# Optimization experiments

Hardware: AMD Instinct MI355X
Metric: run time of the kernel (lower is better)

The kernel has to match this reference:

```python
import jax, jax.numpy as jnp
import numpy as np

PI = 3.141592653589793

# ---------------- smoothing-constant solvers (numpy, import time) -------------
# Quadratic smoothing b*(r-rc)^2 matched to value V and slope dV at r.
def _smooth(V, dV, r):
    rc = r - 2.0 * V / dV
    b = dV * dV / (4.0 * V)
    return float(b), float(rc)

def _f1c(a, r0, rc, rlow, rhigh):  # smoothed Morse (stacking / hbond radial)
    shift = (1.0 - np.exp(-a * (rc - r0))) ** 2
    def V(r):
        return (1.0 - np.exp(-a * (r - r0))) ** 2 - shift
    def dV(r):
        e = np.exp(-a * (r - r0))
        return 2.0 * (1.0 - e) * a * e
    blow, rclow = _smooth(V(rlow), dV(rlow), rlow)
    bhigh, rchigh = _smooth(V(rhigh), dV(rhigh), rhigh)
    return dict(a=a, r0=r0, shift=float(shift), rlow=rlow, rhigh=rhigh,
                blow=blow, rclow=rclow, bhigh=bhigh, rchigh=rchigh)

def _f2c(k, r0, rc, rlow, rhigh):  # smoothed harmonic well (cross/coaxial radial)
    dc2 = (rc - r0) ** 2
    def V(r):
        return 0.5 * k * ((r - r0) ** 2 - dc2)
    def dV(r):
        return k * (r - r0)
    blow, rclow = _smooth(V(rlow), dV(rlow), rlow)
    bhigh, rchigh = _smooth(V(rhigh), dV(rhigh), rhigh)
    return dict(k=k, r0=r0, dc2=float(dc2), rlow=rlow, rhigh=rhigh,
                blow=blow, rclow=rclow, bhigh=bhigh, rchigh=rchigh)

def _f3c(sigma, rstar):  # smoothed LJ excluded volume
    s6 = sigma ** 6
    V = 4.0 * (s6 * s6 / rstar ** 12 - s6 / rstar ** 6)
    dV = 4.0 * (-12.0 * s6 * s6 / rstar ** 13 + 6.0 * s6 / rstar ** 7)
    b, rc = _smooth(V, dV, rstar)
    return dict(sigma=sigma, rstar=rstar, b=b, rc=rc)

def _f4c(a, t0, ts):  # smoothed angular modulation 1-a*(th-t0)^2
    b = a * a * ts * ts / (1.0 - a * ts * ts)
    tc = ts + a * ts / b
    return dict(a=a, t0=t0, ts=ts, b=float(b), tc=float(tc))

def _f5c(a, xs):  # one-sided smoothed modulation on a cosine
    V = 1.0 - a * xs * xs
    dV = -2.0 * a * xs
    xc = xs - 2.0 * V / dV
    b = dV * dV / (4.0 * V)
    return dict(a=a, xs=xs, xc=float(xc), b=float(b))

FENE_EPS, FENE_R0, FENE_DELTA = 2.0, 0.7525, 0.25
F1_STCK = _f1c(6.0, 0.4, 0.9, 0.32, 0.75)
F1_HB = _f1c(8.0, 0.4, 0.75, 0.34, 0.70)
F2_CRST = _f2c(47.5, 0.575, 0.675, 0.495, 0.655)
F2_CX = _f2c(46.0, 0.4, 0.6, 0.22, 0.58)
F3_BACK = _f3c(0.70, 0.675)
F3_BASE = _f3c(0.33, 0.32)
F3_MIX = _f3c(0.515, 0.50)
F4 = dict(
    s4=_f4c(1.30, 0.0, 0.80), s5=_f4c(0.90, 0.0, 0.95), s6=_f4c(0.90, 0.0, 0.95),
    h1=_f4c(1.50, 0.0, 0.70), h2=_f4c(1.50, 0.0, 0.70), h3=_f4c(1.50, 0.0, 0.70),
    h4=_f4c(0.46, PI, 0.70), h7=_f4c(4.00, 0.5 * PI, 0.45), h8=_f4c(4.00, 0.5 * PI, 0.45),
    c1=_f4c(2.25, 0.791, 0.58), c2=_f4c(1.70, 1.003, 0.68), c3=_f4c(1.70, 1.003, 0.68),
    c4=_f4c(1.50, 0.0, 0.70), c7=_f4c(1.70, 0.555, 0.68), c8=_f4c(1.70, 0.555, 0.68),
    x1=_f4c(2.00, 2.592, 0.65), x4=_f4c(1.30, 0.0, 0.80))
F5C = _f5c(2.0, -0.65)
POS_BACK, POS_STACK, POS_BASE = -0.4, 0.34, 0.4

# ---------------- jnp piecewise potential pieces ------------------------------
def f1(r, c):
    e = jnp.exp(-c['a'] * (r - c['r0']))
    core = (1.0 - e) ** 2 - c['shift']
    v = jnp.where(r < c['rlow'], c['blow'] * (r - c['rclow']) ** 2,
        jnp.where(r < c['rhigh'], core, c['bhigh'] * (r - c['rchigh']) ** 2))
    return jnp.where((r > c['rclow']) & (r < c['rchigh']), v, 0.0)

def f2(r, c):
    core = 0.5 * c['k'] * ((r - c['r0']) ** 2 - c['dc2'])
    v = jnp.where(r < c['rlow'], c['blow'] * (r - c['rclow']) ** 2,
        jnp.where(r < c['rhigh'], core, c['bhigh'] * (r - c['rchigh']) ** 2))
    return jnp.where((r > c['rclow']) & (r < c['rchigh']), v, 0.0)

def f3(r, c, eps):
    x6 = (c['sigma'] / r) ** 6
    lj = 4.0 * (x6 * x6 - x6)
    v = jnp.where(r < c['rstar'], lj, c['b'] * (r - c['rc']) ** 2)
    return eps * jnp.where(r < c['rc'], v, 0.0)

def f4(theta, c):
    dt = jnp.abs(theta - c['t0'])
    v = jnp.where(dt < c['ts'], 1.0 - c['a'] * dt * dt, c['b'] * (c['tc'] - dt) ** 2)
    return jnp.where(dt < c['tc'], v, 0.0)

def f5(x, c):
    v = jnp.where(x > c['xs'], 1.0 - c['a'] * x * x, c['b'] * (c['xc'] - x) ** 2)
    v = jnp.where(x > 0.0, 1.0, v)
    return jnp.where(x > c['xc'], v, 0.0)

# ---------------- geometry helpers --------------------------------------------
def quat_axes(q):  # rotation-matrix rows a1,a2,a3, each (N,3)
    w, x, y, z = q[..., 0], q[..., 1], q[..., 2], q[..., 3]
    a1 = jnp.stack([w*w + x*x - y*y - z*z, 2*(x*y + w*z), 2*(x*z - w*y)], -1)
    a2 = jnp.stack([2*(x*y - w*z), w*w - x*x + y*y - z*z, 2*(y*z + w*x)], -1)
    a3 = jnp.stack([2*(x*z + w*y), 2*(y*z - w*x), w*w - x*x - y*y + z*z], -1)
    return a1, a2, a3

def min_image(d, box):
    return d - box * jnp.round(d / box)

def vnorm(d):
    return jnp.sqrt(jnp.sum(d * d, -1) + 1e-12)

def acos(c):
    return jnp.arccos(jnp.clip(c, -1.0 + 1e-6, 1.0 - 1e-6))

def dot(a, b):
    return jnp.sum(a * b, -1)

# ---------------- total oxDNA energy ------------------------------------------
def total_energy(positions, quaternions, box, stacking_eps, hbond_eps_matrix,
                 excl_eps, bonded_pairs, nonbonded_pairs, base_types):
    a1, a2, a3 = quat_axes(quaternions)
    back, stck, base = POS_BACK * a1, POS_STACK * a1, POS_BASE * a1
    bi, bj = bonded_pairs[:, 0], bonded_pairs[:, 1]
    ni, nj = nonbonded_pairs[:, 0], nonbonded_pairs[:, 1]

    def disp(si, sj, i, j):  # min-image site-to-site displacement, (P,3)
        return min_image((positions[j] + sj[j]) - (positions[i] + si[i]), box)

    # FENE (bonded backbone sites)
    rb = vnorm(disp(back, back, bi, bj))
    arg = jnp.clip(((rb - FENE_R0) / FENE_DELTA) ** 2, 0.0, 1.0 - 1e-6)
    e_fene = jnp.sum(-0.5 * FENE_EPS * jnp.log1p(-arg))

    # bonded excluded volume (base-base, back-base, base-back)
    e_bexc = jnp.sum(f3(vnorm(disp(base, base, bi, bj)), F3_BASE, excl_eps)
                     + f3(vnorm(disp(back, base, bi, bj)), F3_MIX, excl_eps)
                     + f3(vnorm(disp(base, back, bi, bj)), F3_MIX, excl_eps))

    # stacking (bonded stacking sites)
    ds = disp(stck, stck, bi, bj)
    rs = vnorm(ds)
    rhs = ds / rs[:, None]
    a3i, a3j, a2i, a2j = a3[bi], a3[bj], a2[bi], a2[bj]
    db = disp(back, back, bi, bj)
    rhb = db / vnorm(db)[:, None]
    th4, th5, th6 = acos(dot(a3i, a3j)), acos(dot(rhs, a3j)), acos(-dot(rhs, a3i))
    e_stck = jnp.sum(stacking_eps * f1(rs, F1_STCK)
                     * f4(th4, F4['s4']) * f4(th5, F4['s5']) * f4(th6, F4['s6'])
                     * f5(dot(a2i, rhb), F5C) * f5(dot(a2j, rhb), F5C))

    # nonbonded gathered frames
    A1i, A1j, A2i, A2j, A3i, A3j = a1[ni], a1[nj], a2[ni], a2[nj], a3[ni], a3[nj]

    # nonbonded excluded volume (all 4 site combos)
    e_nexc = jnp.sum(f3(vnorm(disp(back, back, ni, nj)), F3_BACK, excl_eps)
                     + f3(vnorm(disp(base, base, ni, nj)), F3_BASE, excl_eps)
                     + f3(vnorm(disp(back, base, ni, nj)), F3_MIX, excl_eps)
                     + f3(vnorm(disp(base, back, ni, nj)), F3_MIX, excl_eps))

    # hydrogen bonding (base sites)
    dh = disp(base, base, ni, nj)
    rh = vnorm(dh)
    rhh = dh / rh[:, None]
    t1, t2, t3 = acos(-dot(A1i, A1j)), acos(-dot(rhh, A1j)), acos(dot(rhh, A1i))
    t4, t7, t8 = acos(dot(A3i, A3j)), acos(-dot(rhh, A3j)), acos(dot(rhh, A3i))
    eps_hb = hbond_eps_matrix[base_types[ni], base_types[nj]]
    e_hb = jnp.sum(eps_hb * f1(rh, F1_HB)
                   * f4(t1, F4['h1']) * f4(t2, F4['h2']) * f4(t3, F4['h3'])
                   * f4(t4, F4['h4']) * f4(t7, F4['h7']) * f4(t8, F4['h8']))

    # cross stacking (base sites, same angles)
    e_cr = jnp.sum(f2(rh, F2_CRST)
                   * f4(t1, F4['c1']) * f4(t2, F4['c2']) * f4(t3, F4['c3'])
                   * f4(t4, F4['c4']) * f4(t7, F4['c7']) * f4(t8, F4['c8']))

    # coaxial stacking (stack sites)
    dx = disp(stck, stck, ni, nj)
    rx = vnorm(dx)
    rhx = dx / rx[:, None]
    e_cx = jnp.sum(f2(rx, F2_CX)
                   * f4(acos(-dot(A1i, A1j)), F4['x1']) * f4(acos(dot(A3i, A3j)), F4['x4'])
                   * f5(dot(A2i, rhx), F5C) * f5(dot(A2j, rhx), F5C))

    return e_fene + e_bexc + e_stck + e_nexc + e_hb + e_cr + e_cx


def setup_inputs() -> dict:
    N = 65536
    M = 16 * N
    k = jax.random.split(jax.random.key(0), 6)
    # random-walk chain: bonded neighbours land near the FENE minimum
    steps = jax.random.normal(k[0], (N, 3), dtype=jnp.float32)
    steps = 0.65 * steps / jnp.linalg.norm(steps, axis=-1, keepdims=True)
    positions = jnp.cumsum(steps, axis=0)
    q = jax.random.normal(k[1], (N, 4), dtype=jnp.float32)
    quaternions = q / jnp.linalg.norm(q, axis=-1, keepdims=True)
    box = jnp.full((3,), 200.0, dtype=jnp.float32)
    idx = jnp.arange(N - 1, dtype=jnp.int32)
    bonded_pairs = jnp.stack([idx, idx + 1], axis=1)
    i = jax.random.randint(k[2], (M,), 0, N - 8, dtype=jnp.int32)
    off = jax.random.randint(k[3], (M,), 2, 9, dtype=jnp.int32)
    nonbonded_pairs = jnp.stack([i, i + off], axis=1)  # near-in-chain => inside cutoffs
    base_types = jax.random.randint(k[4], (N,), 0, 4, dtype=jnp.int32)
    stacking_eps = 1.3 + 0.1 * jax.random.uniform(k[5], (N - 1,), dtype=jnp.float32)
    hb = np.zeros((4, 4), dtype=np.float32)  # A=0,C=1,G=2,T=3; only WC pairs bind
    hb[0, 3] = hb[3, 0] = hb[1, 2] = hb[2, 1] = 1.077
    return dict(positions=positions, quaternions=quaternions, box=box,
                stacking_eps=stacking_eps, hbond_eps_matrix=jnp.asarray(hb),
                excl_eps=jnp.float32(2.0), bonded_pairs=bonded_pairs,
                nonbonded_pairs=nonbonded_pairs, base_types=base_types)


def reference(positions, quaternions, box, stacking_eps, hbond_eps_matrix,
              excl_eps, bonded_pairs, nonbonded_pairs, base_types):
    return total_energy(positions, quaternions, box, stacking_eps,
                        hbond_eps_matrix, excl_eps,
                        bonded_pairs, nonbonded_pairs, base_types)
```

## Files before the change

kernel.cpp:

```cpp
#include <hip/hip_runtime.h>
#include <cmath>

#define DEV __device__ __forceinline__

struct F1C { float a, r0, shift, rlow, rhigh, blow, rclow, bhigh, rchigh; };
struct F2C { float k, r0, dc2, rlow, rhigh, blow, rclow, bhigh, rchigh; };
struct F3C { float sigma2, rstar2, b, rc, rc2; };
struct F4C { float a, t0, ts, b, tc; };
struct F5P { float a, xs, xc, b; };

struct Params {
  F1C f1_stck, f1_hb;
  F2C f2_crst, f2_cx;
  F3C f3_back, f3_base, f3_mix;
  F4C s4, s5, h1, h4, h7, c1, c2, c7, x1;
  F5P f5;
  float nlo1sq, nhi1sq, nlo2sq, nhi2sq;
};

DEV float asqrt(float x) { return __builtin_amdgcn_sqrtf(x); }
DEV float arcp(float x)  { return __builtin_amdgcn_rcpf(x); }
DEV float arsq(float x)  { return __builtin_amdgcn_rsqf(x); }

struct V3 { float x, y, z; };
DEV V3 operator+(V3 a, V3 b) { return {a.x + b.x, a.y + b.y, a.z + b.z}; }
DEV V3 operator-(V3 a, V3 b) { return {a.x - b.x, a.y - b.y, a.z - b.z}; }
DEV V3 operator*(float s, V3 a) { return {s * a.x, s * a.y, s * a.z}; }
DEV float dot(V3 a, V3 b) { return a.x * b.x + a.y * b.y + a.z * b.z; }

DEV V3 mim(V3 d, V3 box, V3 ibox) {
  return { d.x - box.x * rintf(d.x * ibox.x),
           d.y - box.y * rintf(d.y * ibox.y),
           d.z - box.z * rintf(d.z * ibox.z) };
}

DEV void quat_a1(float4 q, V3& a1) {
  float w = q.x, x = q.y, y = q.z, z = q.w;
  a1 = { w*w + x*x - y*y - z*z, 2.f*(x*y + w*z), 2.f*(x*z - w*y) };
}

DEV void quat_a23(float4 q, V3& a2, V3& a3) {
  float w = q.x, x = q.y, y = q.z, z = q.w;
  a2 = { 2.f*(x*y - w*z), w*w - x*x + y*y - z*z, 2.f*(y*z + w*x) };
  a3 = { 2.f*(x*z + w*y), 2.f*(y*z - w*x), w*w - x*x - y*y + z*z };
}

DEV float acosc(float x) {
  x = fminf(fmaxf(x, -0.999999f), 0.999999f);
  float u = fabsf(x);
  float p = -0.0012624911f;
  p = fmaf(p, u,  0.0066700901f);
  p = fmaf(p, u, -0.0170881256f);
  p = fmaf(p, u,  0.0308918810f);
  p = fmaf(p, u, -0.0501743046f);
  p = fmaf(p, u,  0.0889789874f);
  p = fmaf(p, u, -0.2145988016f);
  p = fmaf(p, u,  1.5707963050f);
  float r = asqrt(1.f - u) * p;
  return x >= 0.f ? r : 3.14159265358979f - r;
}

DEV float f1f(float r, const F1C& c) {
  if (r <= c.rclow || r >= c.rchigh) return 0.f;
  if (r < c.rlow) { float d = r - c.rclow; return c.blow * d * d; }
  if (r < c.rhigh) {
    float ex = __expf(-c.a * (r - c.r0));
    float t = 1.f - ex;
    return t * t - c.shift;
  }
  float d = r - c.rchigh; return c.bhigh * d * d;
}

DEV float f2f(float r, const F2C& c) {
  if (r <= c.rclow || r >= c.rchigh) return 0.f;
  if (r < c.rlow) { float d = r - c.rclow; return c.blow * d * d; }
  if (r < c.rhigh) { float d = r - c.r0; return 0.5f * c.k * (d * d - c.dc2); }
  float d = r - c.rchigh; return c.bhigh * d * d;
}

DEV float f3f(float r2, const F3C& c, float eps) {
  if (r2 >= c.rc2) return 0.f;
  float v;
  if (r2 < c.rstar2) {
    float t = c.sigma2 * arcp(r2);
    float x6 = t * t * t;
    v = 4.f * (x6 * x6 - x6);
  } else {
    float d = asqrt(r2) - c.rc; v = c.b * d * d;
  }
  return eps * v;
}

DEV float f4f(float th, const F4C& c) {
  float dt = fabsf(th - c.t0);
  if (dt >= c.tc) return 0.f;
  if (dt < c.ts) return 1.f - c.a * dt * dt;
  float d = c.tc - dt; return c.b * d * d;
}

DEV float f5f(float x, const F5P& c) {
  if (x <= c.xc) return 0.f;
  if (x > 0.f) return 1.f;
  if (x > c.xs) return 1.f - c.a * x * x;
  float d = c.xc - x; return c.b * d * d;
}

__global__ void __launch_bounds__(256)
energy_kernel(const float* __restrict__ pos,
              const float4* __restrict__ quat,
              const float* __restrict__ boxp,
              const float* __restrict__ seps,
              const float* __restrict__ hbm,
              const float* __restrict__ exclp,
              const int2* __restrict__ bp,
              const int2* __restrict__ nbp,
              const int* __restrict__ btype,
              int M, int NP, Params P,
              double* __restrict__ partials)
{
  int gid = blockIdx.x * 256 + threadIdx.x;
  float bx = boxp[0], by = boxp[1], bz = boxp[2];
  V3 box = { bx, by, bz };
  V3 ibox = { arcp(bx), arcp(by), arcp(bz) };

  float e = 0.f;
  bool need = false;
  int2 myij = {0, 0};
  if (gid < M + NP) {
    bool isNB = gid < M;
    myij = isNB ? nbp[gid] : bp[gid - M];
    float excl = exclp[0];

    const float* pi_ = pos + 3 * myij.x;
    const float* pj_ = pos + 3 * myij.y;
    V3 dp = { pj_[0] - pi_[0], pj_[1] - pi_[1], pj_[2] - pi_[2] };
    float4 qi = quat[myij.x], qj = quat[myij.y];
    V3 a1i, a1j;
    quat_a1(qi, a1i);
    quat_a1(qj, a1j);

    V3 s = a1j - a1i;
    V3 t = a1j + a1i;
    V3 dbb = mim(dp - 0.4f  * s, box, ibox);
    V3 dhh = mim(dp + 0.4f  * s, box, ibox);
    V3 dbB = mim(dp + 0.4f  * t, box, ibox);
    V3 dBb = mim(dp - 0.4f  * t, box, ibox);
    V3 dss = mim(dp + 0.34f * s, box, ibox);

    float rbb2 = dot(dbb, dbb) + 1e-12f;
    float rhh2 = dot(dhh, dhh) + 1e-12f;
    float rbB2 = dot(dbB, dbB) + 1e-12f;
    float rBb2 = dot(dBb, dBb) + 1e-12f;
    float rss2 = dot(dss, dss) + 1e-12f;

    e += f3f(rhh2, P.f3_base, excl);
    e += f3f(rbB2, P.f3_mix,  excl);
    e += f3f(rBb2, P.f3_mix,  excl);

    if (isNB) {
      e += f3f(rbb2, P.f3_back, excl);
      need = (rhh2 > P.nlo1sq && rhh2 < P.nhi1sq) ||
             (rss2 > P.nlo2sq && rss2 < P.nhi2sq);
    } else {
      float rsbb = arsq(rbb2);
      float rbb  = rbb2 * rsbb;
      float u = (rbb - 0.7525f) * 4.0f;
      float arg = fminf(u * u, 0.999999f);
      e += -__logf(1.f - arg);
      float rsss = arsq(rss2);
      float rss  = rss2 * rsss;
      float f1v = f1f(rss, P.f1_stck);
      if (f1v != 0.f) {
        V3 a2i, a3i, a2j, a3j;
        quat_a23(qi, a2i, a3i);
        quat_a23(qj, a2j, a3j);
        V3 rhs = rsss * dss;
        V3 rhb = rsbb * dbb;
        float th4 = acosc( dot(a3i, a3j));
        float th5 = acosc( dot(rhs, a3j));
        float th6 = acosc(-dot(rhs, a3i));
        e += seps[gid - M] * f1v * f4f(th4, P.s4) * f4f(th5, P.s5) * f4f(th6, P.s5)
                           * f5f(dot(a2i, rhb), P.f5) * f5f(dot(a2j, rhb), P.f5);
      }
    }
  }

  __shared__ unsigned wcnt[4];
  __shared__ int2 spair[256];
  int lane = threadIdx.x & 63, wid = threadIdx.x >> 6;
  unsigned long long mask = __ballot(need);
  if (lane == 0) wcnt[wid] = (unsigned)__popcll(mask);
  __syncthreads();
  unsigned base = 0;
  #pragma unroll
  for (int w = 0; w < 4; ++w) if (w < wid) base += wcnt[w];
  unsigned total = wcnt[0] + wcnt[1] + wcnt[2] + wcnt[3];
  if (need) {
    unsigned pfx = (unsigned)__popcll(mask & ((1ull << lane) - 1ull));
    spair[base + pfx] = myij;
  }
  __syncthreads();

  for (unsigned t = threadIdx.x; t < total; t += 256) {
    int2 ij = spair[t];
    const float* pi_ = pos + 3 * ij.x;
    const float* pj_ = pos + 3 * ij.y;
    V3 dp = { pj_[0] - pi_[0], pj_[1] - pi_[1], pj_[2] - pi_[2] };
    float4 qi = quat[ij.x], qj = quat[ij.y];
    V3 a1i, a2i, a3i, a1j, a2j, a3j;
    quat_a1(qi, a1i);  quat_a23(qi, a2i, a3i);
    quat_a1(qj, a1j);  quat_a23(qj, a2j, a3j);
    V3 s = a1j - a1i;
    V3 dhh = mim(dp + 0.4f  * s, box, ibox);
    V3 dss = mim(dp + 0.34f * s, box, ibox);
    float rhh2 = dot(dhh, dhh) + 1e-12f;
    float rss2 = dot(dss, dss) + 1e-12f;
    float rsh = arsq(rhh2);
    float rhh = rhh2 * rsh;

    float t1 = acosc(-dot(a1i, a1j));
    float t4 = acosc( dot(a3i, a3j));

    V3 rh = rsh * dhh;
    float t2 = acosc(-dot(rh, a1j));
    float t3 = acosc( dot(rh, a1i));
    float t7 = acosc(-dot(rh, a3j));
    float t8 = acosc( dot(rh, a3i));

    float f1v = f1f(rhh, P.f1_hb);
    if (f1v != 0.f) {
      float eps = hbm[btype[ij.x] * 4 + btype[ij.y]];
      e += eps * f1v * f4f(t1, P.h1) * f4f(t2, P.h1) * f4f(t3, P.h1)
               * f4f(t4, P.h4) * f4f(t7, P.h7) * f4f(t8, P.h7);
    }
    float f2v = f2f(rhh, P.f2_crst);
    if (f2v != 0.f)
      e += f2v * f4f(t1, P.c1) * f4f(t2, P.c2) * f4f(t3, P.c2)
               * f4f(t4, P.h1) * f4f(t7, P.c7) * f4f(t8, P.c7);

    float rsx = arsq(rss2);
    float rss = rss2 * rsx;
    float f2x = f2f(rss, P.f2_cx);
    if (f2x != 0.f) {
      V3 rx = rsx * dss;
      e += f2x * f4f(t1, P.x1) * f4f(t4, P.s4)
               * f5f(dot(a2i, rx), P.f5) * f5f(dot(a2j, rx), P.f5);
    }
  }

  double v = (double)e;
  #pragma unroll
  for (int off = 32; off > 0; off >>= 1) v += __shfl_down(v, off, 64);
  __shared__ double sm[4];
  if (lane == 0) sm[wid] = v;
  __syncthreads();
  if (threadIdx.x == 0) partials[blockIdx.x] = sm[0] + sm[1] + sm[2] + sm[3];
}

__global__ void __launch_bounds__(1024)
finalize_kernel(const double* __restrict__ part, int n, float* __restrict__ out) {
  double v = 0.0;
  for (int i = threadIdx.x; i < n; i += 1024) v += part[i];
  #pragma unroll
  for (int off = 32; off > 0; off >>= 1) v += __shfl_down(v, off, 64);
  __shared__ double sm[16];
  int lane = threadIdx.x & 63, wid = threadIdx.x >> 6;
  if (lane == 0) sm[wid] = v;
  __syncthreads();
  if (wid == 0) {
    v = (lane < 16) ? sm[lane] : 0.0;
    #pragma unroll
    for (int off = 8; off > 0; off >>= 1) v += __shfl_down(v, off, 64);
    if (lane == 0) out[0] = (float)v;
  }
}

static inline double sqd(double x) { return x * x; }

static F1C mkf1(double a, double r0, double rc, double rlow, double rhigh) {
  double shift = sqd(1.0 - exp(-a * (rc - r0)));
  double el = exp(-a * (rlow - r0)), eh = exp(-a * (rhigh - r0));
  double Vl = sqd(1.0 - el) - shift, Vh = sqd(1.0 - eh) - shift;
  double dVl = 2.0 * (1.0 - el) * a * el, dVh = 2.0 * (1.0 - eh) * a * eh;
  double rclow = rlow - 2.0 * Vl / dVl, blow = dVl * dVl / (4.0 * Vl);
  double rchigh = rhigh - 2.0 * Vh / dVh, bhigh = dVh * dVh / (4.0 * Vh);
  return { (float)a, (float)r0, (float)shift, (float)rlow, (float)rhigh,
           (float)blow, (float)rclow, (float)bhigh, (float)rchigh };
}

static F2C mkf2(double k, double r0, double rc, double rlow, double rhigh) {
  double dc2 = sqd(rc - r0);
  double Vl = 0.5 * k * (sqd(rlow - r0) - dc2), Vh = 0.5 * k * (sqd(rhigh - r0) - dc2);
  double dVl = k * (rlow - r0), dVh = k * (rhigh - r0);
  double rclow = rlow - 2.0 * Vl / dVl, blow = dVl * dVl / (4.0 * Vl);
  double rchigh = rhigh - 2.0 * Vh / dVh, bhigh = dVh * dVh / (4.0 * Vh);
  return { (float)k, (float)r0, (float)dc2, (float)rlow, (float)rhigh,
           (float)blow, (float)rclow, (float)bhigh, (float)rchigh };
}

static F3C mkf3(double sigma, double rstar) {
  double s6 = pow(sigma, 6.0);
  double V = 4.0 * (s6 * s6 / pow(rstar, 12.0) - s6 / pow(rstar, 6.0));
  double dV = 4.0 * (-12.0 * s6 * s6 / pow(rstar, 13.0) + 6.0 * s6 / pow(rstar, 7.0));
  double rc = rstar - 2.0 * V / dV, b = dV * dV / (4.0 * V);
  return { (float)(sigma * sigma), (float)(rstar * rstar), (float)b,
           (float)rc, (float)(rc * rc) };
}

static F4C mkf4(double a, double t0, double ts) {
  double b = a * a * ts * ts / (1.0 - a * ts * ts);
  double tc = ts + a * ts / b;
  return { (float)a, (float)t0, (float)ts, (float)b, (float)tc };
}

static F5P mkf5(double a, double xs) {
  double V = 1.0 - a * xs * xs, dV = -2.0 * a * xs;
  double xc = xs - 2.0 * V / dV, b = dV * dV / (4.0 * V);
  return { (float)a, (float)xs, (float)xc, (float)b };
}

extern "C" void kernel_launch(void* const* d_in, const int* in_sizes, int n_in,
                              void* d_out, int out_size, void* d_ws, size_t ws_size,
                              hipStream_t stream) {
  (void)n_in; (void)out_size; (void)ws_size;
  const double PI = 3.141592653589793;

  const float*  pos  = (const float*)d_in[0];
  const float4* quat = (const float4*)d_in[1];
  const float*  box  = (const float*)d_in[2];
  const float*  seps = (const float*)d_in[3];
  const float*  hbm  = (const float*)d_in[4];
  const float*  excl = (const float*)d_in[5];
  const int2*   bp   = (const int2*)d_in[6];
  const int2*   nbp  = (const int2*)d_in[7];
  const int*    bt   = (const int*)d_in[8];

  int NP = in_sizes[6] / 2;
  int M  = in_sizes[7] / 2;
  int total = M + NP;
  int blocks = (total + 255) / 256;

  Params P;
  P.f1_stck = mkf1(6.0, 0.4, 0.9, 0.32, 0.75);
  P.f1_hb   = mkf1(8.0, 0.4, 0.75, 0.34, 0.7);
  P.f2_crst = mkf2(47.5, 0.575, 0.675, 0.495, 0.655);
  P.f2_cx   = mkf2(46.0, 0.4, 0.6, 0.22, 0.58);
  P.f3_back = mkf3(0.7, 0.675);
  P.f3_base = mkf3(0.33, 0.32);
  P.f3_mix  = mkf3(0.515, 0.5);
  P.s4 = mkf4(1.3, 0.0, 0.8);
  P.s5 = mkf4(0.9, 0.0, 0.95);
  P.h1 = mkf4(1.5, 0.0, 0.7);
  P.h4 = mkf4(0.46, PI, 0.7);
  P.h7 = mkf4(4.0, 0.5 * PI, 0.45);
  P.c1 = mkf4(2.25, 0.791, 0.58);
  P.c2 = mkf4(1.7, 1.003, 0.68);
  P.c7 = mkf4(1.7, 0.555, 0.68);
  P.x1 = mkf4(2.0, 2.592, 0.65);
  P.f5 = mkf5(2.0, -0.65);
  {
    double lo1 = (double)P.f1_hb.rclow  - 1e-3, hi1 = (double)P.f1_hb.rchigh + 1e-3;
    double lo2 = (double)P.f2_cx.rclow  - 1e-3, hi2 = (double)P.f2_cx.rchigh + 1e-3;
    P.nlo1sq = (float)(lo1 * lo1);  P.nhi1sq = (float)(hi1 * hi1);
    P.nlo2sq = (float)(lo2 * lo2);  P.nhi2sq = (float)(hi2 * hi2);
  }

  double* partials = (double*)d_ws;

  energy_kernel<<<blocks, 256, 0, stream>>>(pos, quat, box, seps, hbm, excl,
                                            bp, nbp, bt, M, NP, P, partials);
  finalize_kernel<<<1, 1024, 0, stream>>>(partials, blocks, (float*)d_out);
}
```

Measured before the change: 110.0 us.

## Pack positions, quaternions and base types into per-particle float4 records

Adds a pre-pass kernel that interleaves each particle's position, base type and quaternion into two adjacent float4s in workspace. The energy kernel then fetches each particle with two 16-byte gathers instead of three scalar position loads, a quaternion load and separate base-type loads. This aims to cut scattered memory transactions in the gather-heavy pair loop, at the cost of an extra kernel launch and a full pass over the particle data. It also assumes the packed records fit in the first 4 MiB of workspace.

```diff
diff --git a/kernel.cpp b/kernel.cpp
--- a/kernel.cpp
+++ b/kernel.cpp
@@ -106,15 +106,26 @@
 }
 
 __global__ void __launch_bounds__(256)
-energy_kernel(const float* __restrict__ pos,
-              const float4* __restrict__ quat,
+pack_kernel(const float* __restrict__ pos,
+            const float4* __restrict__ quat,
+            const int* __restrict__ btype,
+            int N, float4* __restrict__ rec)
+{
+  int i = blockIdx.x * 256 + threadIdx.x;
+  if (i < N) {
+    rec[2*i]   = { pos[3*i], pos[3*i+1], pos[3*i+2], __int_as_float(btype[i]) };
+    rec[2*i+1] = quat[i];
+  }
+}
+
+__global__ void __launch_bounds__(256)
+energy_kernel(const float4* __restrict__ rec,
               const float* __restrict__ boxp,
               const float* __restrict__ seps,
               const float* __restrict__ hbm,
               const float* __restrict__ exclp,
               const int2* __restrict__ bp,
               const int2* __restrict__ nbp,
-              const int* __restrict__ btype,
               int M, int NP, Params P,
               double* __restrict__ partials)
 {
@@ -131,10 +142,9 @@
     myij = isNB ? nbp[gid] : bp[gid - M];
     float excl = exclp[0];
 
-    const float* pi_ = pos + 3 * myij.x;
-    const float* pj_ = pos + 3 * myij.y;
-    V3 dp = { pj_[0] - pi_[0], pj_[1] - pi_[1], pj_[2] - pi_[2] };
-    float4 qi = quat[myij.x], qj = quat[myij.y];
+    float4 pi4 = rec[2*myij.x], qi = rec[2*myij.x+1];
+    float4 pj4 = rec[2*myij.y], qj = rec[2*myij.y+1];
+    V3 dp = { pj4.x - pi4.x, pj4.y - pi4.y, pj4.z - pi4.z };
     V3 a1i, a1j;
     quat_a1(qi, a1i);
     quat_a1(qj, a1j);
@@ -203,10 +213,9 @@
 
   for (unsigned t = threadIdx.x; t < total; t += 256) {
     int2 ij = spair[t];
-    const float* pi_ = pos + 3 * ij.x;
-    const float* pj_ = pos + 3 * ij.y;
-    V3 dp = { pj_[0] - pi_[0], pj_[1] - pi_[1], pj_[2] - pi_[2] };
-    float4 qi = quat[ij.x], qj = quat[ij.y];
+    float4 pi4 = rec[2*ij.x], qi = rec[2*ij.x+1];
+    float4 pj4 = rec[2*ij.y], qj = rec[2*ij.y+1];
+    V3 dp = { pj4.x - pi4.x, pj4.y - pi4.y, pj4.z - pi4.z };
     V3 a1i, a2i, a3i, a1j, a2j, a3j;
     quat_a1(qi, a1i);  quat_a23(qi, a2i, a3i);
     quat_a1(qj, a1j);  quat_a23(qj, a2j, a3j);
@@ -229,7 +238,8 @@
 
     float f1v = f1f(rhh, P.f1_hb);
     if (f1v != 0.f) {
-      float eps = hbm[btype[ij.x] * 4 + btype[ij.y]];
+      int bti = __float_as_int(pi4.w), btj = __float_as_int(pj4.w);
+      float eps = hbm[bti * 4 + btj];
       e += eps * f1v * f4f(t1, P.h1) * f4f(t2, P.h1) * f4f(t3, P.h1)
                * f4f(t4, P.h4) * f4f(t7, P.h7) * f4f(t8, P.h7);
     }
@@ -335,6 +345,7 @@
   const int2*   nbp  = (const int2*)d_in[7];
   const int*    bt   = (const int*)d_in[8];
 
+  int N  = in_sizes[0] / 3;
   int NP = in_sizes[6] / 2;
   int M  = in_sizes[7] / 2;
   int total = M + NP;
@@ -365,9 +376,11 @@
     P.nlo2sq = (float)(lo2 * lo2);  P.nhi2sq = (float)(hi2 * hi2);
   }
 
-  double* partials = (double*)d_ws;
-
-  energy_kernel<<<blocks, 256, 0, stream>>>(pos, quat, box, seps, hbm, excl,
-                                            bp, nbp, bt, M, NP, P, partials);
+  float4* rec       = (float4*)d_ws;
+  double* partials  = (double*)((char*)d_ws + (4u << 20));
+
+  pack_kernel<<<(N + 255) / 256, 256, 0, stream>>>(pos, quat, bt, N, rec);
+  energy_kernel<<<blocks, 256, 0, stream>>>(rec, box, seps, hbm, excl,
+                                            bp, nbp, M, NP, P, partials);
   finalize_kernel<<<1, 1024, 0, stream>>>(partials, blocks, (float*)d_out);
 }
```

After: 106.1 us. -3.6%, faster.
